# Performance work log

Measured on AMD Instinct MI355X. Metric: run time of the kernel, lower is better.

## Reference

```python
import jax, jax.numpy as jnp
import numpy as np

B, T, V, E, H, O = 32, 512, 32000, 512, 1024, 128


def setup_inputs() -> dict:
    key = jax.random.key(0)
    ks = jax.random.split(key, 8)
    s = lambda k, shape: (jax.random.normal(k, shape) * 0.02).astype(jnp.float32)
    return {
        "tokens": jax.random.randint(ks[0], (B, T), 0, V),
        "verb_indices": jax.random.randint(ks[1], (B,), 0, T),
        "emb": s(ks[2], (V, E)),
        "W_ih": s(ks[3], (4 * H, E)),
        "W_hh": s(ks[4], (4 * H, H)),
        "b_ih": jnp.zeros((4 * H,), jnp.float32),
        "b_hh": jnp.zeros((4 * H,), jnp.float32),
        "W_lin": s(ks[5], (O, 2 * H)),
        "b_lin": jnp.zeros((O,), jnp.float32),
    }


def _lstm(e, W_ih, W_hh, b_ih, b_hh):
    # e: [B,T,E] -> hidden states [B,T,H]; PyTorch gate order i,f,g,o
    Hd = W_hh.shape[1]
    # precompute input projections for all timesteps (one big GEMM)
    x_proj = jnp.einsum("bte,ge->btg", e, W_ih) + b_ih + b_hh  # [B,T,4H]

    def step(carry, x_t):
        h, c = carry
        gates = x_t + h @ W_hh.T  # [B,4H]
        i, f, g, o = jnp.split(gates, 4, axis=-1)
        i = jax.nn.sigmoid(i)
        f = jax.nn.sigmoid(f)
        g = jnp.tanh(g)
        o = jax.nn.sigmoid(o)
        c = f * c + i * g
        h = o * jnp.tanh(c)
        return (h, c), h

    h0 = jnp.zeros((e.shape[0], Hd), e.dtype)
    (_, _), hs = jax.lax.scan(step, (h0, h0), jnp.swapaxes(x_proj, 0, 1))
    return jnp.swapaxes(hs, 0, 1)  # [B,T,H]


def reference(tokens, verb_indices, emb, W_ih, W_hh, b_ih, b_hh, W_lin, b_lin):
    e = emb[tokens]  # [B,T,E]
    out = _lstm(e, W_ih, W_hh, b_ih, b_hh)  # [B,T,H]
    verbs = out[jnp.arange(out.shape[0]), verb_indices]  # [B,H] verb hidden state
    # linear over concat([verb, out_t]) == split the weight and sum two GEMMs
    Wv, Wo = jnp.split(W_lin, 2, axis=1)  # [O,H] each
    logits = (
        jnp.einsum("bh,oh->bo", verbs, Wv)[:, None, :]
        + jnp.einsum("bth,oh->bto", out, Wo)
        + b_lin
    )  # [B,T,O]
    return jax.nn.log_softmax(logits, axis=-1)
```

## Files before the change

kernel.cpp:

```cpp
#include <hip/hip_runtime.h>


typedef short s8v __attribute__((ext_vector_type(8)));
typedef float f4v __attribute__((ext_vector_type(4)));

#define WS_CNT_OFF   131072
#define WS_VROWS_OFF 139264
#define WS_VLOG_OFF  204800

__device__ __forceinline__ float b2f(unsigned short u) {
    union { unsigned int i; float f; } x; x.i = ((unsigned int)u) << 16; return x.f;
}
__device__ __forceinline__ unsigned short f2b(float f) {
    union { float f; unsigned int i; } x; x.f = f;
    unsigned int r = (x.i + 0x7fffu + ((x.i >> 16) & 1u)) >> 16;
    return (unsigned short)r;
}
__device__ __forceinline__ float blo(unsigned int u) {
    union { unsigned int i; float f; } x; x.i = u << 16; return x.f;
}
__device__ __forceinline__ float bhi(unsigned int u) {
    union { unsigned int i; float f; } x; x.i = u & 0xffff0000u; return x.f;
}

__global__ void init_kernel(unsigned int* ws) {
    int i = blockIdx.x * 256 + threadIdx.x;
    if (i < 34816) ws[i] = 0u;
}

__device__ __forceinline__ void project_cols(
    const short* hA, const float* __restrict__ Wr0, const float* __restrict__ Wr1,
    float* __restrict__ dout, int b0, int tproj, int w, int tid)
{
    const int pair = tid >> 4, p = tid & 15;
    const int b = pair >> 1, oc = pair & 1;
    const float* wr = oc ? Wr1 : Wr0;
    float acc = 0.f;
#pragma unroll
    for (int j = 0; j < 8; ++j) {
        int ko = j * 16 + p;
        const unsigned int* d = (const unsigned int*)&hA[(ko * 17 + b) * 8];
        const float* wk = wr + ko * 8;
        f4v w0 = *(const f4v*)wk, w1 = *(const f4v*)(wk + 4);
        unsigned int d0 = d[0], d1 = d[1], d2 = d[2], d3 = d[3];
        acc += blo(d0) * w0[0] + bhi(d0) * w0[1] + blo(d1) * w0[2] + bhi(d1) * w0[3]
             + blo(d2) * w1[0] + bhi(d2) * w1[1] + blo(d3) * w1[2] + bhi(d3) * w1[3];
    }
#pragma unroll
    for (int off = 1; off < 16; off <<= 1) acc += __shfl_xor(acc, off);
    if (p == 0)
        dout[((size_t)(b0 + b) * 512 + tproj) * 128 + 2 * w + oc] = acc;
}

__global__ __launch_bounds__(256, 1) void scan_kernel(
    const int* __restrict__ tokens,
    const int* __restrict__ vidx,
    const float* __restrict__ emb,
    const float* __restrict__ W_ih,
    const float* __restrict__ W_hh,
    const float* __restrict__ b_ih,
    const float* __restrict__ b_hh,
    const float* __restrict__ W_lin,
    unsigned short* __restrict__ hbuf,
    unsigned int* __restrict__ cnt,
    unsigned short* __restrict__ vrows,
    float* __restrict__ dout)
{
    __shared__ short hA[128 * 17 * 8];
    __shared__ short eA[64 * 17 * 8];
    __shared__ float gbuf[16 * 65];

    const int tid  = threadIdx.x;
    const int g    = blockIdx.x >> 6;
    const int w    = blockIdx.x & 63;
    const int b0   = g * 8;
    const int lane = tid & 63;
    const int v    = tid >> 6;
    const int q    = lane >> 4;
    const int c    = lane & 15;

    const float* Wr0 = W_lin + (size_t)(2 * w) * 2048 + 1024;
    const float* Wr1 = W_lin + (size_t)(2 * w + 1) * 2048 + 1024;

    const int n = ((c >> 2) * 1024) + 16 * w + 4 * v + (c & 3);
    s8v Bh[32], Be[16];
    {
        const float* rh = W_hh + (size_t)n * 1024;
#pragma unroll
        for (int ks = 0; ks < 32; ++ks) {
            const float* s = rh + ks * 32 + q * 8;
            f4v lo = *(const f4v*)s, hi = *(const f4v*)(s + 4);
            s8v f;
#pragma unroll
            for (int j = 0; j < 4; ++j) { f[j] = (short)f2b(lo[j]); f[j + 4] = (short)f2b(hi[j]); }
            Bh[ks] = f;
        }
        const float* re = W_ih + (size_t)n * 512;
#pragma unroll
        for (int ks = 0; ks < 16; ++ks) {
            const float* s = re + ks * 32 + q * 8;
            f4v lo = *(const f4v*)s, hi = *(const f4v*)(s + 4);
            s8v f;
#pragma unroll
            for (int j = 0; j < 4; ++j) { f[j] = (short)f2b(lo[j]); f[j + 4] = (short)f2b(hi[j]); }
            Be[ks] = f;
        }
    }

    const s8v zv = {0,0,0,0,0,0,0,0};
    for (int i = tid; i < 1024; i += 256) { int ko = i >> 3, r = 8 + (i & 7);
        *(s8v*)&hA[(ko * 17 + r) * 8] = zv; }
    for (int i = tid; i < 512; i += 256) { int ko = i >> 3, r = 8 + (i & 7);
        *(s8v*)&eA[(ko * 17 + r) * 8] = zv; }

    float cst0 = 0.f, cst1 = 0.f;
    float bi0 = 0, bf0 = 0, bg0 = 0, bo0 = 0, bi1 = 0, bf1 = 0, bg1 = 0, bo1 = 0;
    int tvb = -1;
    const int pb = tid >> 3, pj2 = tid & 7;
    if (tid < 64) {
        int n0 = 16 * w + 2 * pj2, n1 = n0 + 1;
        bi0 = b_ih[n0]        + b_hh[n0];        bi1 = b_ih[n1]        + b_hh[n1];
        bf0 = b_ih[1024 + n0] + b_hh[1024 + n0]; bf1 = b_ih[1024 + n1] + b_hh[1024 + n1];
        bg0 = b_ih[2048 + n0] + b_hh[2048 + n0]; bg1 = b_ih[2048 + n1] + b_hh[2048 + n1];
        bo0 = b_ih[3072 + n0] + b_hh[3072 + n0]; bo1 = b_ih[3072 + n1] + b_hh[3072 + n1];
        tvb = vidx[b0 + pb];
    }

    unsigned short* hb   = hbuf + g * 2 * 8192;
    unsigned int*   hb32 = (unsigned int*)hb;
    unsigned int*   mycnt = cnt + g * 512;
    const int dwidx = ((2 * w + (pj2 >> 2)) * 8 + pb) * 4 + (pj2 & 3);
    int rp = 0;
    __syncthreads();

    for (int t = 0; t < 512; ++t) {
        for (int i = tid; i < 512; i += 256) {
            int ko = i >> 3, b = i & 7;
            int tok = tokens[(b0 + b) * 512 + t];
            const float* s = emb + (size_t)tok * 512 + ko * 8;
            f4v lo = *(const f4v*)s, hi = *(const f4v*)(s + 4);
            s8v f;
#pragma unroll
            for (int j = 0; j < 4; ++j) { f[j] = (short)f2b(lo[j]); f[j + 4] = (short)f2b(hi[j]); }
            *(s8v*)&eA[(ko * 17 + b) * 8] = f;
        }

        if (t >= 2)
            project_cols(hA, Wr0, Wr1, dout, b0, t - 2, w, tid);

        __syncthreads();

        f4v ae = {0.f, 0.f, 0.f, 0.f};
#pragma unroll
        for (int ks = 0; ks < 16; ++ks) {
            s8v a = *(const s8v*)&eA[((ks * 4 + q) * 17 + c) * 8];
            ae = __builtin_amdgcn_mfma_f32_16x16x32_bf16(a, Be[ks], ae, 0, 0, 0);
        }

        if (t > 0) {
            while (__hip_atomic_load(&mycnt[t - 1], __ATOMIC_RELAXED,
                                     __HIP_MEMORY_SCOPE_AGENT) < 64u) {}
        }

        {
            const unsigned long long* src =
                (const unsigned long long*)(hb + rp * 8192);
#pragma unroll
            for (int it = 0; it < 8; ++it) {
                int j = it * 256 + tid;
                unsigned long long d = __hip_atomic_load(src + j, __ATOMIC_RELAXED,
                                                         __HIP_MEMORY_SCOPE_AGENT);
                int ko = j >> 4, b = (j >> 1) & 7, posq = (j & 1) << 2;
                *(unsigned long long*)&hA[(ko * 17 + b) * 8 + posq] = d;
            }
        }
        __syncthreads();

        f4v ah0 = {0.f, 0.f, 0.f, 0.f}, ah1 = {0.f, 0.f, 0.f, 0.f};
#pragma unroll
        for (int ks = 0; ks < 16; ++ks) {
            s8v a0 = *(const s8v*)&hA[((2 * ks) * 4 + q) * 17 * 8 + c * 8];
            s8v a1 = *(const s8v*)&hA[((2 * ks + 1) * 4 + q) * 17 * 8 + c * 8];
            ah0 = __builtin_amdgcn_mfma_f32_16x16x32_bf16(a0, Bh[2 * ks], ah0, 0, 0, 0);
            ah1 = __builtin_amdgcn_mfma_f32_16x16x32_bf16(a1, Bh[2 * ks + 1], ah1, 0, 0, 0);
        }

#pragma unroll
        for (int r = 0; r < 4; ++r)
            gbuf[(q * 4 + r) * 65 + v * 16 + c] = ae[r] + ah0[r] + ah1[r];
        __syncthreads();

        if (tid < 64) {
            float h0, h1;
            {
                int pj = 2 * pj2, base = (pj >> 2) * 16, cb = pj & 3;
                float xi = gbuf[pb * 65 + base + cb]      + bi0;
                float xf = gbuf[pb * 65 + base + 4 + cb]  + bf0;
                float xg = gbuf[pb * 65 + base + 8 + cb]  + bg0;
                float xo = gbuf[pb * 65 + base + 12 + cb] + bo0;
                float ig = 1.f / (1.f + __expf(-xi));
                float fg = 1.f / (1.f + __expf(-xf));
                float gg = 1.f - 2.f / (1.f + __expf(2.f * xg));
                float og = 1.f / (1.f + __expf(-xo));
                cst0 = fg * cst0 + ig * gg;
                h0 = og * (1.f - 2.f / (1.f + __expf(2.f * cst0)));
            }
            {
                int pj = 2 * pj2 + 1, base = (pj >> 2) * 16, cb = pj & 3;
                float xi = gbuf[pb * 65 + base + cb]      + bi1;
                float xf = gbuf[pb * 65 + base + 4 + cb]  + bf1;
                float xg = gbuf[pb * 65 + base + 8 + cb]  + bg1;
                float xo = gbuf[pb * 65 + base + 12 + cb] + bo1;
                float ig = 1.f / (1.f + __expf(-xi));
                float fg = 1.f / (1.f + __expf(-xf));
                float gg = 1.f - 2.f / (1.f + __expf(2.f * xg));
                float og = 1.f / (1.f + __expf(-xo));
                cst1 = fg * cst1 + ig * gg;
                h1 = og * (1.f - 2.f / (1.f + __expf(2.f * cst1)));
            }
            unsigned int pack = (unsigned int)f2b(h0) | ((unsigned int)f2b(h1) << 16);
            __hip_atomic_store(&hb32[(rp ^ 1) * 4096 + dwidx], pack,
                               __ATOMIC_RELAXED, __HIP_MEMORY_SCOPE_AGENT);
            if (t == tvb)
                *(unsigned int*)&vrows[(b0 + pb) * 1024 + 16 * w + 2 * pj2] = pack;
        }
        __syncthreads();

        if (tid == 0)
            __hip_atomic_fetch_add(&mycnt[t], 1u, __ATOMIC_RELAXED,
                                   __HIP_MEMORY_SCOPE_AGENT);
        rp ^= 1;
    }

    project_cols(hA, Wr0, Wr1, dout, b0, 510, w, tid);
    __syncthreads();
    while (__hip_atomic_load(&mycnt[511], __ATOMIC_RELAXED,
                             __HIP_MEMORY_SCOPE_AGENT) < 64u) {}
    {
        const unsigned long long* src = (const unsigned long long*)(hb + rp * 8192);
#pragma unroll
        for (int it = 0; it < 8; ++it) {
            int j = it * 256 + tid;
            unsigned long long d = __hip_atomic_load(src + j, __ATOMIC_RELAXED,
                                                     __HIP_MEMORY_SCOPE_AGENT);
            int ko = j >> 4, b = (j >> 1) & 7, posq = (j & 1) << 2;
            *(unsigned long long*)&hA[(ko * 17 + b) * 8 + posq] = d;
        }
    }
    __syncthreads();
    project_cols(hA, Wr0, Wr1, dout, b0, 511, w, tid);
}

__global__ void verb_kernel(const unsigned short* __restrict__ vrows,
                            const float* __restrict__ W_lin,
                            const float* __restrict__ b_lin,
                            float* __restrict__ vlog)
{
    __shared__ float vrow[1024];
    int b = blockIdx.x, tid = threadIdx.x;
    for (int i = tid; i < 1024; i += 256) vrow[i] = b2f(vrows[b * 1024 + i]);
    __syncthreads();
    if (tid < 128) {
        float acc = 0.f;
        const float* wr = W_lin + (size_t)tid * 2048;
        for (int h = 0; h < 1024; ++h) acc += vrow[h] * wr[h];
        vlog[b * 128 + tid] = acc + b_lin[tid];
    }
}

__global__ void softmax_kernel(float* __restrict__ dout,
                               const float* __restrict__ vlog)
{
    int tid = threadIdx.x;
    int grow = blockIdx.x * 32 + (tid >> 3);
    int part = tid & 7;
    int b = grow >> 9;
    float* pp = dout + (size_t)grow * 128 + part * 16;
    const float* vb = vlog + b * 128 + part * 16;
    float L[16];
#pragma unroll
    for (int i = 0; i < 16; ++i) L[i] = pp[i] + vb[i];
    float m = L[0];
#pragma unroll
    for (int i = 1; i < 16; ++i) m = fmaxf(m, L[i]);
    for (int off = 1; off < 8; off <<= 1) m = fmaxf(m, __shfl_xor(m, off));
    float s = 0.f;
#pragma unroll
    for (int i = 0; i < 16; ++i) s += expf(L[i] - m);
    for (int off = 1; off < 8; off <<= 1) s += __shfl_xor(s, off);
    float lz = m + logf(s);
#pragma unroll
    for (int i = 0; i < 16; ++i) pp[i] = L[i] - lz;
}

extern "C" void kernel_launch(void* const* d_in, const int* in_sizes, int n_in,
                              void* d_out, int out_size, void* d_ws, size_t ws_size,
                              hipStream_t stream) {
    const int*   tokens = (const int*)d_in[0];
    const int*   vidx   = (const int*)d_in[1];
    const float* emb    = (const float*)d_in[2];
    const float* W_ih   = (const float*)d_in[3];
    const float* W_hh   = (const float*)d_in[4];
    const float* b_ih   = (const float*)d_in[5];
    const float* b_hh   = (const float*)d_in[6];
    const float* W_lin  = (const float*)d_in[7];
    const float* b_lin  = (const float*)d_in[8];
    float* dout = (float*)d_out;

    char* ws = (char*)d_ws;
    unsigned short* hbuf  = (unsigned short*)ws;
    unsigned int*   cnt   = (unsigned int*)(ws + WS_CNT_OFF);
    unsigned short* vrows = (unsigned short*)(ws + WS_VROWS_OFF);
    float*          vlog  = (float*)(ws + WS_VLOG_OFF);

    init_kernel<<<136, 256, 0, stream>>>((unsigned int*)ws);
    scan_kernel<<<256, 256, 0, stream>>>(tokens, vidx, emb, W_ih, W_hh, b_ih, b_hh,
                                         W_lin, hbuf, cnt, vrows, dout);
    verb_kernel<<<32, 256, 0, stream>>>(vrows, W_lin, b_lin, vlog);
    softmax_kernel<<<512, 256, 0, stream>>>(dout, vlog);
}
```

Baseline: 3.453 ms.

## Replace per-step atomic counters with per-block flags polled by wavefront ballot

```diff
diff --git a/kernel.cpp b/kernel.cpp
--- a/kernel.cpp
+++ b/kernel.cpp
@@ -4,7 +4,7 @@
 typedef short s8v __attribute__((ext_vector_type(8)));
 typedef float f4v __attribute__((ext_vector_type(4)));
 
-#define WS_CNT_OFF   131072
+#define WS_FLAG_OFF  131072
 #define WS_VROWS_OFF 139264
 #define WS_VLOG_OFF  204800
 
@@ -62,7 +62,7 @@
     const float* __restrict__ b_hh,
     const float* __restrict__ W_lin,
     unsigned short* __restrict__ hbuf,
-    unsigned int* __restrict__ cnt,
+    unsigned int* __restrict__ flags,
     unsigned short* __restrict__ vrows,
     float* __restrict__ dout)
 {
@@ -71,8 +71,8 @@
     __shared__ float gbuf[16 * 65];
 
     const int tid  = threadIdx.x;
-    const int g    = blockIdx.x >> 6;
-    const int w    = blockIdx.x & 63;
+    const int g    = blockIdx.x & 3;
+    const int w    = blockIdx.x >> 2;
     const int b0   = g * 8;
     const int lane = tid & 63;
     const int v    = tid >> 6;
@@ -126,9 +126,9 @@
         tvb = vidx[b0 + pb];
     }
 
-    unsigned short* hb   = hbuf + g * 2 * 8192;
-    unsigned int*   hb32 = (unsigned int*)hb;
-    unsigned int*   mycnt = cnt + g * 512;
+    unsigned short* hb    = hbuf + g * 2 * 8192;
+    unsigned int*   hb32  = (unsigned int*)hb;
+    unsigned int*   myfl  = flags + g * 64;
     const int dwidx = ((2 * w + (pj2 >> 2)) * 8 + pb) * 4 + (pj2 & 3);
     int rp = 0;
     __syncthreads();
@@ -158,8 +158,13 @@
         }
 
         if (t > 0) {
-            while (__hip_atomic_load(&mycnt[t - 1], __ATOMIC_RELAXED,
-                                     __HIP_MEMORY_SCOPE_AGENT) < 64u) {}
+            const unsigned int tgt = (unsigned int)t;
+            for (;;) {
+                unsigned int fv = __hip_atomic_load(&myfl[lane], __ATOMIC_RELAXED,
+                                                    __HIP_MEMORY_SCOPE_AGENT);
+                if (__ballot(fv >= tgt) == ~0ull) break;
+                __builtin_amdgcn_s_sleep(1);
+            }
         }
 
         {
@@ -223,20 +228,23 @@
                                __ATOMIC_RELAXED, __HIP_MEMORY_SCOPE_AGENT);
             if (t == tvb)
                 *(unsigned int*)&vrows[(b0 + pb) * 1024 + 16 * w + 2 * pj2] = pack;
-        }
-        __syncthreads();
-
-        if (tid == 0)
-            __hip_atomic_fetch_add(&mycnt[t], 1u, __ATOMIC_RELAXED,
-                                   __HIP_MEMORY_SCOPE_AGENT);
+            __builtin_amdgcn_s_waitcnt(0);
+            if (tid == 0)
+                __hip_atomic_store(&myfl[w], (unsigned int)(t + 1),
+                                   __ATOMIC_RELAXED, __HIP_MEMORY_SCOPE_AGENT);
+        }
         rp ^= 1;
     }
 
     project_cols(hA, Wr0, Wr1, dout, b0, 510, w, tid);
     __syncthreads();
-    while (__hip_atomic_load(&mycnt[511], __ATOMIC_RELAXED,
-                             __HIP_MEMORY_SCOPE_AGENT) < 64u) {}
     {
+        for (;;) {
+            unsigned int fv = __hip_atomic_load(&myfl[lane], __ATOMIC_RELAXED,
+                                                __HIP_MEMORY_SCOPE_AGENT);
+            if (__ballot(fv >= 512u) == ~0ull) break;
+            __builtin_amdgcn_s_sleep(1);
+        }
         const unsigned long long* src = (const unsigned long long*)(hb + rp * 8192);
 #pragma unroll
         for (int it = 0; it < 8; ++it) {
@@ -309,13 +317,13 @@
 
     char* ws = (char*)d_ws;
     unsigned short* hbuf  = (unsigned short*)ws;
-    unsigned int*   cnt   = (unsigned int*)(ws + WS_CNT_OFF);
+    unsigned int*   flags = (unsigned int*)(ws + WS_FLAG_OFF);
     unsigned short* vrows = (unsigned short*)(ws + WS_VROWS_OFF);
     float*          vlog  = (float*)(ws + WS_VLOG_OFF);
 
     init_kernel<<<136, 256, 0, stream>>>((unsigned int*)ws);
     scan_kernel<<<256, 256, 0, stream>>>(tokens, vidx, emb, W_ih, W_hh, b_ih, b_hh,
-                                         W_lin, hbuf, cnt, vrows, dout);
+                                         W_lin, hbuf, flags, vrows, dout);
     verb_kernel<<<32, 256, 0, stream>>>(vrows, W_lin, b_lin, vlog);
     softmax_kernel<<<512, 256, 0, stream>>>(dout, vlog);
 }
```

After: 3.562 ms. 3.2% more time.

## Replace counter barrier with tagged hidden-state payloads and register-resident gate math

Applied to the files above, without the earlier changes.

```diff
diff --git a/kernel.cpp b/kernel.cpp
--- a/kernel.cpp
+++ b/kernel.cpp
@@ -4,9 +4,8 @@
 typedef short s8v __attribute__((ext_vector_type(8)));
 typedef float f4v __attribute__((ext_vector_type(4)));
 
-#define WS_CNT_OFF   131072
-#define WS_VROWS_OFF 139264
-#define WS_VLOG_OFF  204800
+#define WS_VROWS_OFF 262144
+#define WS_VLOG_OFF  327680
 
 __device__ __forceinline__ float b2f(unsigned short u) {
     union { unsigned int i; float f; } x; x.i = ((unsigned int)u) << 16; return x.f;
@@ -21,11 +20,6 @@
 }
 __device__ __forceinline__ float bhi(unsigned int u) {
     union { unsigned int i; float f; } x; x.i = u & 0xffff0000u; return x.f;
-}
-
-__global__ void init_kernel(unsigned int* ws) {
-    int i = blockIdx.x * 256 + threadIdx.x;
-    if (i < 34816) ws[i] = 0u;
 }
 
 __device__ __forceinline__ void project_cols(
@@ -61,28 +55,27 @@
     const float* __restrict__ b_ih,
     const float* __restrict__ b_hh,
     const float* __restrict__ W_lin,
-    unsigned short* __restrict__ hbuf,
-    unsigned int* __restrict__ cnt,
+    unsigned long long* __restrict__ hbuf,
     unsigned short* __restrict__ vrows,
     float* __restrict__ dout)
 {
     __shared__ short hA[128 * 17 * 8];
     __shared__ short eA[64 * 17 * 8];
-    __shared__ float gbuf[16 * 65];
 
     const int tid  = threadIdx.x;
-    const int g    = blockIdx.x >> 6;
-    const int w    = blockIdx.x & 63;
+    const int g    = blockIdx.x & 3;
+    const int w    = blockIdx.x >> 2;
     const int b0   = g * 8;
     const int lane = tid & 63;
     const int v    = tid >> 6;
     const int q    = lane >> 4;
     const int c    = lane & 15;
+    const int u    = c & 3;
 
     const float* Wr0 = W_lin + (size_t)(2 * w) * 2048 + 1024;
     const float* Wr1 = W_lin + (size_t)(2 * w + 1) * 2048 + 1024;
 
-    const int n = ((c >> 2) * 1024) + 16 * w + 4 * v + (c & 3);
+    const int n = ((c >> 2) * 1024) + 16 * w + 4 * v + u;
     s8v Bh[32], Be[16];
     {
         const float* rh = W_hh + (size_t)n * 1024;
@@ -108,145 +101,126 @@
     }
 
     const s8v zv = {0,0,0,0,0,0,0,0};
-    for (int i = tid; i < 1024; i += 256) { int ko = i >> 3, r = 8 + (i & 7);
-        *(s8v*)&hA[(ko * 17 + r) * 8] = zv; }
-    for (int i = tid; i < 512; i += 256) { int ko = i >> 3, r = 8 + (i & 7);
-        *(s8v*)&eA[(ko * 17 + r) * 8] = zv; }
-
-    float cst0 = 0.f, cst1 = 0.f;
-    float bi0 = 0, bf0 = 0, bg0 = 0, bo0 = 0, bi1 = 0, bf1 = 0, bg1 = 0, bo1 = 0;
-    int tvb = -1;
-    const int pb = tid >> 3, pj2 = tid & 7;
-    if (tid < 64) {
-        int n0 = 16 * w + 2 * pj2, n1 = n0 + 1;
-        bi0 = b_ih[n0]        + b_hh[n0];        bi1 = b_ih[n1]        + b_hh[n1];
-        bf0 = b_ih[1024 + n0] + b_hh[1024 + n0]; bf1 = b_ih[1024 + n1] + b_hh[1024 + n1];
-        bg0 = b_ih[2048 + n0] + b_hh[2048 + n0]; bg1 = b_ih[2048 + n1] + b_hh[2048 + n1];
-        bo0 = b_ih[3072 + n0] + b_hh[3072 + n0]; bo1 = b_ih[3072 + n1] + b_hh[3072 + n1];
-        tvb = vidx[b0 + pb];
-    }
-
-    unsigned short* hb   = hbuf + g * 2 * 8192;
-    unsigned int*   hb32 = (unsigned int*)hb;
-    unsigned int*   mycnt = cnt + g * 512;
-    const int dwidx = ((2 * w + (pj2 >> 2)) * 8 + pb) * 4 + (pj2 & 3);
-    int rp = 0;
-    __syncthreads();
+    for (int i = tid; i < 128 * 17; i += 256) *(s8v*)&hA[i * 8] = zv;
+    for (int i = tid; i < 64 * 17;  i += 256) *(s8v*)&eA[i * 8] = zv;
+
+    float bi, bf, bg, bo;
+    {
+        int n0 = 16 * w + 4 * v + u;
+        bi = b_ih[n0]        + b_hh[n0];
+        bf = b_ih[1024 + n0] + b_hh[1024 + n0];
+        bg = b_ih[2048 + n0] + b_hh[2048 + n0];
+        bo = b_ih[3072 + n0] + b_hh[3072 + n0];
+    }
+    int vr[4];
+#pragma unroll
+    for (int r = 0; r < 4; ++r) vr[r] = vidx[b0 + ((4 * q + r) & 7)];
+    float cst[4] = {0.f, 0.f, 0.f, 0.f};
+
+    unsigned long long* hbq = hbuf + g * 8192;
+
+    for (int i = tid; i < 512; i += 256) {
+        int ko = i >> 3, b = i & 7;
+        int tok = tokens[(b0 + b) * 512 + 0];
+        const float* s = emb + (size_t)tok * 512 + ko * 8;
+        f4v lo = *(const f4v*)s, hi = *(const f4v*)(s + 4);
+        s8v f;
+#pragma unroll
+        for (int j = 0; j < 4; ++j) { f[j] = (short)f2b(lo[j]); f[j + 4] = (short)f2b(hi[j]); }
+        *(s8v*)&eA[(ko * 17 + b) * 8] = f;
+    }
 
     for (int t = 0; t < 512; ++t) {
-        for (int i = tid; i < 512; i += 256) {
-            int ko = i >> 3, b = i & 7;
-            int tok = tokens[(b0 + b) * 512 + t];
-            const float* s = emb + (size_t)tok * 512 + ko * 8;
-            f4v lo = *(const f4v*)s, hi = *(const f4v*)(s + 4);
-            s8v f;
-#pragma unroll
-            for (int j = 0; j < 4; ++j) { f[j] = (short)f2b(lo[j]); f[j + 4] = (short)f2b(hi[j]); }
-            *(s8v*)&eA[(ko * 17 + b) * 8] = f;
-        }
-
-        if (t >= 2)
-            project_cols(hA, Wr0, Wr1, dout, b0, t - 2, w, tid);
-
         __syncthreads();
 
-        f4v ae = {0.f, 0.f, 0.f, 0.f};
+        f4v ae = {0,0,0,0}, ah0 = {0,0,0,0}, ah1 = {0,0,0,0};
 #pragma unroll
         for (int ks = 0; ks < 16; ++ks) {
-            s8v a = *(const s8v*)&eA[((ks * 4 + q) * 17 + c) * 8];
-            ae = __builtin_amdgcn_mfma_f32_16x16x32_bf16(a, Be[ks], ae, 0, 0, 0);
-        }
-
-        if (t > 0) {
-            while (__hip_atomic_load(&mycnt[t - 1], __ATOMIC_RELAXED,
-                                     __HIP_MEMORY_SCOPE_AGENT) < 64u) {}
+            s8v aE  = *(const s8v*)&eA[((ks * 4 + q) * 17 + c) * 8];
+            s8v aH0 = *(const s8v*)&hA[(((2 * ks) * 4 + q) * 17 + c) * 8];
+            s8v aH1 = *(const s8v*)&hA[(((2 * ks + 1) * 4 + q) * 17 + c) * 8];
+            ae  = __builtin_amdgcn_mfma_f32_16x16x32_bf16(aE,  Be[ks],       ae,  0, 0, 0);
+            ah0 = __builtin_amdgcn_mfma_f32_16x16x32_bf16(aH0, Bh[2 * ks],   ah0, 0, 0, 0);
+            ah1 = __builtin_amdgcn_mfma_f32_16x16x32_bf16(aH1, Bh[2 * ks+1], ah1, 0, 0, 0);
+        }
+
+        const unsigned int tagv = (unsigned int)(t + 1);
+        unsigned long long* dstq = hbq + (t & 1) * 4096;
+#pragma unroll
+        for (int r = 0; r < 4; ++r) {
+            float a0 = ae[r] + ah0[r] + ah1[r];
+            float fv = __shfl_xor(a0, 4);
+            float gv = __shfl_xor(a0, 8);
+            float ov = __shfl_xor(fv, 8);
+            float xi = a0 + bi, xf = fv + bf, xg = gv + bg, xo = ov + bo;
+            float ig = 1.f / (1.f + __expf(-xi));
+            float fg = 1.f / (1.f + __expf(-xf));
+            float gt = 1.f - 2.f / (1.f + __expf(2.f * xg));
+            float og = 1.f / (1.f + __expf(-xo));
+            cst[r] = fg * cst[r] + ig * gt;
+            float h = og * (1.f - 2.f / (1.f + __expf(2.f * cst[r])));
+            float hh = __shfl_xor(h, 1);
+            if (q < 2 && (c == 0 || c == 2)) {
+                unsigned int pack = (unsigned int)f2b(h) | ((unsigned int)f2b(hh) << 16);
+                int qidx = (8 * w + 2 * v + (c >> 1)) * 8 + 4 * q + r;
+                __hip_atomic_store(&dstq[qidx],
+                                   (unsigned long long)pack | ((unsigned long long)tagv << 32),
+                                   __ATOMIC_RELAXED, __HIP_MEMORY_SCOPE_AGENT);
+                if (t == vr[r])
+                    *(unsigned int*)&vrows[(b0 + 4 * q + r) * 1024 + 16 * w + 4 * v + c] = pack;
+            }
+        }
+
+        if (t >= 1)
+            project_cols(hA, Wr0, Wr1, dout, b0, t - 1, w, tid);
+
+        __syncthreads();
+
+        if (t < 511) {
+            for (int i = tid; i < 512; i += 256) {
+                int ko = i >> 3, b = i & 7;
+                int tok = tokens[(b0 + b) * 512 + t + 1];
+                const float* s = emb + (size_t)tok * 512 + ko * 8;
+                f4v lo = *(const f4v*)s, hi = *(const f4v*)(s + 4);
+                s8v f;
+#pragma unroll
+                for (int j = 0; j < 4; ++j) { f[j] = (short)f2b(lo[j]); f[j + 4] = (short)f2b(hi[j]); }
+                *(s8v*)&eA[(ko * 17 + b) * 8] = f;
+            }
         }
 
         {
-            const unsigned long long* src =
-                (const unsigned long long*)(hb + rp * 8192);
-#pragma unroll
-            for (int it = 0; it < 8; ++it) {
-                int j = it * 256 + tid;
-                unsigned long long d = __hip_atomic_load(src + j, __ATOMIC_RELAXED,
-                                                         __HIP_MEMORY_SCOPE_AGENT);
-                int ko = j >> 4, b = (j >> 1) & 7, posq = (j & 1) << 2;
-                *(unsigned long long*)&hA[(ko * 17 + b) * 8 + posq] = d;
-            }
-        }
-        __syncthreads();
-
-        f4v ah0 = {0.f, 0.f, 0.f, 0.f}, ah1 = {0.f, 0.f, 0.f, 0.f};
-#pragma unroll
-        for (int ks = 0; ks < 16; ++ks) {
-            s8v a0 = *(const s8v*)&hA[((2 * ks) * 4 + q) * 17 * 8 + c * 8];
-            s8v a1 = *(const s8v*)&hA[((2 * ks + 1) * 4 + q) * 17 * 8 + c * 8];
-            ah0 = __builtin_amdgcn_mfma_f32_16x16x32_bf16(a0, Bh[2 * ks], ah0, 0, 0, 0);
-            ah1 = __builtin_amdgcn_mfma_f32_16x16x32_bf16(a1, Bh[2 * ks + 1], ah1, 0, 0, 0);
-        }
-
-#pragma unroll
-        for (int r = 0; r < 4; ++r)
-            gbuf[(q * 4 + r) * 65 + v * 16 + c] = ae[r] + ah0[r] + ah1[r];
-        __syncthreads();
-
-        if (tid < 64) {
-            float h0, h1;
-            {
-                int pj = 2 * pj2, base = (pj >> 2) * 16, cb = pj & 3;
-                float xi = gbuf[pb * 65 + base + cb]      + bi0;
-                float xf = gbuf[pb * 65 + base + 4 + cb]  + bf0;
-                float xg = gbuf[pb * 65 + base + 8 + cb]  + bg0;
-                float xo = gbuf[pb * 65 + base + 12 + cb] + bo0;
-                float ig = 1.f / (1.f + __expf(-xi));
-                float fg = 1.f / (1.f + __expf(-xf));
-                float gg = 1.f - 2.f / (1.f + __expf(2.f * xg));
-                float og = 1.f / (1.f + __expf(-xo));
-                cst0 = fg * cst0 + ig * gg;
-                h0 = og * (1.f - 2.f / (1.f + __expf(2.f * cst0)));
-            }
-            {
-                int pj = 2 * pj2 + 1, base = (pj >> 2) * 16, cb = pj & 3;
-                float xi = gbuf[pb * 65 + base + cb]      + bi1;
-                float xf = gbuf[pb * 65 + base + 4 + cb]  + bf1;
-                float xg = gbuf[pb * 65 + base + 8 + cb]  + bg1;
-                float xo = gbuf[pb * 65 + base + 12 + cb] + bo1;
-                float ig = 1.f / (1.f + __expf(-xi));
-                float fg = 1.f / (1.f + __expf(-xf));
-                float gg = 1.f - 2.f / (1.f + __expf(2.f * xg));
-                float og = 1.f / (1.f + __expf(-xo));
-                cst1 = fg * cst1 + ig * gg;
-                h1 = og * (1.f - 2.f / (1.f + __expf(2.f * cst1)));
-            }
-            unsigned int pack = (unsigned int)f2b(h0) | ((unsigned int)f2b(h1) << 16);
-            __hip_atomic_store(&hb32[(rp ^ 1) * 4096 + dwidx], pack,
-                               __ATOMIC_RELAXED, __HIP_MEMORY_SCOPE_AGENT);
-            if (t == tvb)
-                *(unsigned int*)&vrows[(b0 + pb) * 1024 + 16 * w + 2 * pj2] = pack;
-        }
-        __syncthreads();
-
-        if (tid == 0)
-            __hip_atomic_fetch_add(&mycnt[t], 1u, __ATOMIC_RELAXED,
-                                   __HIP_MEMORY_SCOPE_AGENT);
-        rp ^= 1;
-    }
-
-    project_cols(hA, Wr0, Wr1, dout, b0, 510, w, tid);
-    __syncthreads();
-    while (__hip_atomic_load(&mycnt[511], __ATOMIC_RELAXED,
-                             __HIP_MEMORY_SCOPE_AGENT) < 64u) {}
-    {
-        const unsigned long long* src = (const unsigned long long*)(hb + rp * 8192);
-#pragma unroll
-        for (int it = 0; it < 8; ++it) {
-            int j = it * 256 + tid;
-            unsigned long long d = __hip_atomic_load(src + j, __ATOMIC_RELAXED,
-                                                     __HIP_MEMORY_SCOPE_AGENT);
-            int ko = j >> 4, b = (j >> 1) & 7, posq = (j & 1) << 2;
-            *(unsigned long long*)&hA[(ko * 17 + b) * 8 + posq] = d;
-        }
-    }
+            const unsigned long long* src = hbq + (t & 1) * 4096;
+            unsigned int pay[16];
+            unsigned int got = 0;
+            while (got != 0xffffu) {
+#pragma unroll
+                for (int i = 0; i < 16; ++i) {
+                    if (!(got & (1u << i))) {
+                        int ri = i >> 2, p = i & 3;
+                        int row = tid + 256 * ri;
+                        int ko = row >> 3, bt = row & 7;
+                        unsigned long long d = __hip_atomic_load(
+                            &src[(4 * ko + p) * 8 + bt],
+                            __ATOMIC_RELAXED, __HIP_MEMORY_SCOPE_AGENT);
+                        if ((unsigned int)(d >> 32) == tagv) {
+                            pay[i] = (unsigned int)d;
+                            got |= (1u << i);
+                        }
+                    }
+                }
+            }
+#pragma unroll
+            for (int ri = 0; ri < 4; ++ri) {
+                int row = tid + 256 * ri, ko = row >> 3, bt = row & 7;
+                union { unsigned int uu[4]; s8v vv; } tmp;
+                tmp.uu[0] = pay[4 * ri];     tmp.uu[1] = pay[4 * ri + 1];
+                tmp.uu[2] = pay[4 * ri + 2]; tmp.uu[3] = pay[4 * ri + 3];
+                *(s8v*)&hA[(ko * 17 + bt) * 8] = tmp.vv;
+            }
+        }
+    }
+
     __syncthreads();
     project_cols(hA, Wr0, Wr1, dout, b0, 511, w, tid);
 }
@@ -308,14 +282,12 @@
     float* dout = (float*)d_out;
 
     char* ws = (char*)d_ws;
-    unsigned short* hbuf  = (unsigned short*)ws;
-    unsigned int*   cnt   = (unsigned int*)(ws + WS_CNT_OFF);
-    unsigned short* vrows = (unsigned short*)(ws + WS_VROWS_OFF);
-    float*          vlog  = (float*)(ws + WS_VLOG_OFF);
-
-    init_kernel<<<136, 256, 0, stream>>>((unsigned int*)ws);
+    unsigned long long* hbuf  = (unsigned long long*)ws;
+    unsigned short*     vrows = (unsigned short*)(ws + WS_VROWS_OFF);
+    float*              vlog  = (float*)(ws + WS_VLOG_OFF);
+
     scan_kernel<<<256, 256, 0, stream>>>(tokens, vidx, emb, W_ih, W_hh, b_ih, b_hh,
-                                         W_lin, hbuf, cnt, vrows, dout);
+                                         W_lin, hbuf, vrows, dout);
     verb_kernel<<<32, 256, 0, stream>>>(vrows, W_lin, b_lin, vlog);
     softmax_kernel<<<512, 256, 0, stream>>>(dout, vlog);
 }
```

New measurement: 4.007 ms. 16.0% more time.
